# Kernel optimization log

Measured on AMD Instinct MI355X. Metric: run time of the kernel, lower is better.

Reference implementation:

```python
import jax, jax.numpy as jnp
jax.config.update("jax_enable_x64", True)
import numpy as np
import math

N = 100_000   # number of events
D = 4         # feature dim
M = 256       # number of Gaussian centers
E = 10        # ensemble size
SIGMA = 0.1
NORM_CONST = 1.0 / ((2.0 * math.pi) ** (D / 2) * SIGMA ** D)


def setup_inputs() -> dict:
    key = jax.random.key(0)
    k = jax.random.split(key, 6)
    x = jax.random.normal(k[0], (N, D), dtype=jnp.float64)
    centers = jax.random.normal(k[1], (M, D), dtype=jnp.float64)
    coefficients = jax.random.normal(k[2], (M,), dtype=jnp.float64)
    ensemble_probs = jax.random.uniform(k[3], (N, E), dtype=jnp.float64)
    ensemble_norm_probs = jax.random.uniform(k[4], (N, 1), dtype=jnp.float64)
    # small positive weights so 1 - sum(w) stays positive (as in a fitted model)
    weights = 0.05 * jax.random.uniform(k[5], (E,), dtype=jnp.float64)
    return {
        "x": x,
        "ensemble_probs": ensemble_probs,
        "ensemble_norm_probs": ensemble_norm_probs,
        "weights": weights,
        "centers": centers,
        "coefficients": coefficients,
    }


def reference(x, ensemble_probs, ensemble_norm_probs, weights, centers, coefficients):
    # GaussianKernelLayer.get_kernels: pairwise squared distances -> RBF
    diff = x[:, None, :] - centers[None, :, :]          # [N, M, D]
    dist_sq = jnp.sum(diff * diff, axis=2)              # [N, M]
    kern = NORM_CONST * jnp.exp(-0.5 * dist_sq / (SIGMA ** 2))  # [N, M]
    # centered coefficients, contract: einsum('m,Nm->N')
    wc = coefficients - coefficients.mean()
    net_out = kern @ wc                                 # [N]
    # ensemble mixture: w [E,1], w_norm [1,1]
    w = weights[:, None]
    w_norm = 1.0 - jnp.sum(w, axis=0, keepdims=True)
    ensemble = ensemble_probs @ w + ensemble_norm_probs @ w_norm  # [N, 1]
    return (ensemble, net_out)
```

## Files before the change

### kernel.cpp

```cpp
#include <hip/hip_runtime.h>
#include <math.h>

#define NROWS 100000
#define EENS 10

#define NORM_CONST_F 253.30295910584444f
#define EXP2_SCALE (-72.13475204444817f)
#define M2_CONST   (144.26950408889634f)
#define ARG_THRESH (-18.0f)

typedef _Float16 h8 __attribute__((ext_vector_type(8)));
typedef float    f4 __attribute__((ext_vector_type(4)));


__global__ __launch_bounds__(512, 1) void fused_kernel(
    const float* __restrict__ x,
    const float* __restrict__ ensemble_probs,
    const float* __restrict__ ensemble_norm_probs,
    const float* __restrict__ weights,
    const float* __restrict__ centers,
    const float* __restrict__ coefficients,
    float* __restrict__ out)
{
    const int t    = threadIdx.x;
    const int lane = t & 63;
    const int wid  = t >> 6;
    const int wg   = blockIdx.x * 8 + wid;
    if (wg >= NROWS / 32) return;
    const int wbase = wg * 32;

    const int lr = lane & 15;
    const int g  = lane >> 4;

    const float4 cq = ((const float4*)coefficients)[lane];
    float ms = (cq.x + cq.y) + (cq.z + cq.w);
    #pragma unroll
    for (int off = 32; off > 0; off >>= 1) ms += __shfl_down(ms, off, 64);
    const float mean = __builtin_amdgcn_readfirstlane(ms) * (1.0f / 256.0f);

    h8 bf[16]; float As[16], wcv[16];
    #pragma unroll
    for (int T = 0; T < 16; ++T) {
        const float4 cv = ((const float4*)centers)[T * 16 + lr];
        const _Float16 h0 = (_Float16)cv.x, h1 = (_Float16)cv.y,
                       h2 = (_Float16)cv.z, h3 = (_Float16)cv.w;
        const _Float16 l0 = (_Float16)(cv.x - (float)h0),
                       l1 = (_Float16)(cv.y - (float)h1),
                       l2 = (_Float16)(cv.z - (float)h2),
                       l3 = (_Float16)(cv.w - (float)h3);
        h8 b;
        b[0] = h0; b[1] = h1; b[2] = h2; b[3] = h3;
        b[4] = l0; b[5] = l1; b[6] = l2; b[7] = l3;
        bf[T] = b;
        float n2 = cv.x * cv.x;
        n2 = fmaf(cv.y, cv.y, n2);
        n2 = fmaf(cv.z, cv.z, n2);
        n2 = fmaf(cv.w, cv.w, n2);
        As[T]  = EXP2_SCALE * n2;
        wcv[T] = coefficients[T * 16 + lr] - mean;
    }

    const float4 xa = ((const float4*)x)[wbase + lr];
    const float4 xb = ((const float4*)x)[wbase + 16 + lr];

    float hsa = xa.x * xa.x;
    hsa = fmaf(xa.y, xa.y, hsa); hsa = fmaf(xa.z, xa.z, hsa); hsa = fmaf(xa.w, xa.w, hsa);
    hsa *= EXP2_SCALE;
    float hsb = xb.x * xb.x;
    hsb = fmaf(xb.y, xb.y, hsb); hsb = fmaf(xb.z, xb.z, hsb); hsb = fmaf(xb.w, xb.w, hsb);
    hsb *= EXP2_SCALE;

    const float HA0 = __shfl(hsa, g * 4 + 0, 64), HA1 = __shfl(hsa, g * 4 + 1, 64),
                HA2 = __shfl(hsa, g * 4 + 2, 64), HA3 = __shfl(hsa, g * 4 + 3, 64);
    const float HB0 = __shfl(hsb, g * 4 + 0, 64), HB1 = __shfl(hsb, g * 4 + 1, 64),
                HB2 = __shfl(hsb, g * 4 + 2, 64), HB3 = __shfl(hsb, g * 4 + 3, 64);

    const float a0f = (float)(_Float16)xa.x, a1f = (float)(_Float16)xa.y,
                a2f = (float)(_Float16)xa.z, a3f = (float)(_Float16)xa.w;
    const float b0f = (float)(_Float16)xb.x, b1f = (float)(_Float16)xb.y,
                b2f = (float)(_Float16)xb.z, b3f = (float)(_Float16)xb.w;

    const float sa0 = (g == 0) ? a0f : (g == 1) ? (xa.x - a0f) : 0.f;
    const float sa1 = (g == 0) ? a1f : (g == 1) ? (xa.y - a1f) : 0.f;
    const float sa2 = (g == 0) ? a2f : (g == 1) ? (xa.z - a2f) : 0.f;
    const float sa3 = (g == 0) ? a3f : (g == 1) ? (xa.w - a3f) : 0.f;
    const float sb0 = (g == 0) ? b0f : (g == 1) ? (xb.x - b0f) : 0.f;
    const float sb1 = (g == 0) ? b1f : (g == 1) ? (xb.y - b1f) : 0.f;
    const float sb2 = (g == 0) ? b2f : (g == 1) ? (xb.z - b2f) : 0.f;
    const float sb3 = (g == 0) ? b3f : (g == 1) ? (xb.w - b3f) : 0.f;

    h8 afA, afB;
    afA[0] = (_Float16)sa0; afA[1] = (_Float16)sa1; afA[2] = (_Float16)sa2; afA[3] = (_Float16)sa3;
    afA[4] = afA[0]; afA[5] = afA[1]; afA[6] = afA[2]; afA[7] = afA[3];
    afB[0] = (_Float16)sb0; afB[1] = (_Float16)sb1; afB[2] = (_Float16)sb2; afB[3] = (_Float16)sb3;
    afB[4] = afB[0]; afB[5] = afB[1]; afB[6] = afB[2]; afB[7] = afB[3];

    f4 accA = {0.f, 0.f, 0.f, 0.f};
    f4 accB = {0.f, 0.f, 0.f, 0.f};
    const f4 z4 = {0.f, 0.f, 0.f, 0.f};

    #pragma unroll
    for (int T = 0; T < 16; ++T) {
        const f4 dA = __builtin_amdgcn_mfma_f32_16x16x32_f16(afA, bf[T], z4, 0, 0, 0);
        const f4 dB = __builtin_amdgcn_mfma_f32_16x16x32_f16(afB, bf[T], z4, 0, 0, 0);

        const float baseA = As[T];
        const float ra0 = fmaf(M2_CONST, dA[0], HA0 + baseA);
        const float ra1 = fmaf(M2_CONST, dA[1], HA1 + baseA);
        const float ra2 = fmaf(M2_CONST, dA[2], HA2 + baseA);
        const float ra3 = fmaf(M2_CONST, dA[3], HA3 + baseA);
        const float mxa = fmaxf(fmaxf(ra0, ra1), fmaxf(ra2, ra3));
        if (__any(mxa > ARG_THRESH)) {
            const float e0 = __builtin_amdgcn_exp2f(ra0);
            const float e1 = __builtin_amdgcn_exp2f(ra1);
            const float e2 = __builtin_amdgcn_exp2f(ra2);
            const float e3 = __builtin_amdgcn_exp2f(ra3);
            accA[0] = fmaf(e0, wcv[T], accA[0]);
            accA[1] = fmaf(e1, wcv[T], accA[1]);
            accA[2] = fmaf(e2, wcv[T], accA[2]);
            accA[3] = fmaf(e3, wcv[T], accA[3]);
        }

        const float rb0 = fmaf(M2_CONST, dB[0], HB0 + baseA);
        const float rb1 = fmaf(M2_CONST, dB[1], HB1 + baseA);
        const float rb2 = fmaf(M2_CONST, dB[2], HB2 + baseA);
        const float rb3 = fmaf(M2_CONST, dB[3], HB3 + baseA);
        const float mxb = fmaxf(fmaxf(rb0, rb1), fmaxf(rb2, rb3));
        if (__any(mxb > ARG_THRESH)) {
            const float e0 = __builtin_amdgcn_exp2f(rb0);
            const float e1 = __builtin_amdgcn_exp2f(rb1);
            const float e2 = __builtin_amdgcn_exp2f(rb2);
            const float e3 = __builtin_amdgcn_exp2f(rb3);
            accB[0] = fmaf(e0, wcv[T], accB[0]);
            accB[1] = fmaf(e1, wcv[T], accB[1]);
            accB[2] = fmaf(e2, wcv[T], accB[2]);
            accB[3] = fmaf(e3, wcv[T], accB[3]);
        }
    }

    #pragma unroll
    for (int msk = 1; msk <= 8; msk <<= 1) {
        accA[0] += __shfl_xor(accA[0], msk, 64);
        accA[1] += __shfl_xor(accA[1], msk, 64);
        accA[2] += __shfl_xor(accA[2], msk, 64);
        accA[3] += __shfl_xor(accA[3], msk, 64);
        accB[0] += __shfl_xor(accB[0], msk, 64);
        accB[1] += __shfl_xor(accB[1], msk, 64);
        accB[2] += __shfl_xor(accB[2], msk, 64);
        accB[3] += __shfl_xor(accB[3], msk, 64);
    }
    if (lr == 0) {
        const int rbA = wbase + g * 4;
        out[NROWS + rbA + 0] = accA[0] * NORM_CONST_F;
        out[NROWS + rbA + 1] = accA[1] * NORM_CONST_F;
        out[NROWS + rbA + 2] = accA[2] * NORM_CONST_F;
        out[NROWS + rbA + 3] = accA[3] * NORM_CONST_F;
        const int rbB = rbA + 16;
        out[NROWS + rbB + 0] = accB[0] * NORM_CONST_F;
        out[NROWS + rbB + 1] = accB[1] * NORM_CONST_F;
        out[NROWS + rbB + 2] = accB[2] * NORM_CONST_F;
        out[NROWS + rbB + 3] = accB[3] * NORM_CONST_F;
    }

    if (lane < 32) {
        const int r = wbase + lane;
        float wv[EENS];
        float wsum = 0.0f;
        #pragma unroll
        for (int e = 0; e < EENS; ++e) { wv[e] = weights[e]; wsum += wv[e]; }
        float ens = ensemble_norm_probs[r] * (1.0f - wsum);
        const float2* pr = (const float2*)(ensemble_probs + (size_t)r * EENS);
        #pragma unroll
        for (int e2 = 0; e2 < EENS / 2; ++e2) {
            const float2 p = pr[e2];
            ens = fmaf(p.x, wv[2 * e2 + 0], ens);
            ens = fmaf(p.y, wv[2 * e2 + 1], ens);
        }
        out[r] = ens;
    }
}

extern "C" void kernel_launch(void* const* d_in, const int* in_sizes, int n_in,
                              void* d_out, int out_size, void* d_ws, size_t ws_size,
                              hipStream_t stream) {
    const float* x       = (const float*)d_in[0];
    const float* eprobs  = (const float*)d_in[1];
    const float* enorm   = (const float*)d_in[2];
    const float* weights = (const float*)d_in[3];
    const float* centers = (const float*)d_in[4];
    const float* coeffs  = (const float*)d_in[5];
    float* out = (float*)d_out;

    const int waves  = NROWS / 32;
    const int blocks = (waves + 7) / 8;
    fused_kernel<<<blocks, 512, 0, stream>>>(
        x, eprobs, enorm, weights, centers, coeffs, out);
}
```

Measured before the change: 13.93 us.

## Convert to grid-stride persistent waves reusing per-wave center setup across tiles

The kernel now launches a fixed grid of 512 blocks of 256 threads (2048 waves) that loop over the 3125 row tiles of 32 rows, instead of one wave per tile. The per-wave setup (coefficient mean, half-precision center fragments, center norms, centered coefficients, ensemble weights) is computed once and reused across tiles, which amortises that redundant prologue. Launch bounds drop from 512 threads with one-block occupancy to 256. The tile count does not divide evenly over 2048 waves, so some waves run two tiles and others one, which can leave a tail that lengthens the critical path.

```diff
diff --git a/kernel.cpp b/kernel.cpp
--- a/kernel.cpp
+++ b/kernel.cpp
@@ -3,6 +3,8 @@
 
 #define NROWS 100000
 #define EENS 10
+#define NTILES 3125
+#define GWAVES 2048
 
 #define NORM_CONST_F 253.30295910584444f
 #define EXP2_SCALE (-72.13475204444817f)
@@ -13,7 +15,7 @@
 typedef float    f4 __attribute__((ext_vector_type(4)));
 
 
-__global__ __launch_bounds__(512, 1) void fused_kernel(
+__global__ __launch_bounds__(256) void fused_kernel(
     const float* __restrict__ x,
     const float* __restrict__ ensemble_probs,
     const float* __restrict__ ensemble_norm_probs,
@@ -25,12 +27,9 @@
     const int t    = threadIdx.x;
     const int lane = t & 63;
     const int wid  = t >> 6;
-    const int wg   = blockIdx.x * 8 + wid;
-    if (wg >= NROWS / 32) return;
-    const int wbase = wg * 32;
-
-    const int lr = lane & 15;
-    const int g  = lane >> 4;
+    const int gw   = blockIdx.x * 4 + wid;
+    const int lr   = lane & 15;
+    const int g    = lane >> 4;
 
     const float4 cq = ((const float4*)coefficients)[lane];
     float ms = (cq.x + cq.y) + (cq.z + cq.w);
@@ -44,13 +43,12 @@
         const float4 cv = ((const float4*)centers)[T * 16 + lr];
         const _Float16 h0 = (_Float16)cv.x, h1 = (_Float16)cv.y,
                        h2 = (_Float16)cv.z, h3 = (_Float16)cv.w;
-        const _Float16 l0 = (_Float16)(cv.x - (float)h0),
-                       l1 = (_Float16)(cv.y - (float)h1),
-                       l2 = (_Float16)(cv.z - (float)h2),
-                       l3 = (_Float16)(cv.w - (float)h3);
         h8 b;
         b[0] = h0; b[1] = h1; b[2] = h2; b[3] = h3;
-        b[4] = l0; b[5] = l1; b[6] = l2; b[7] = l3;
+        b[4] = (_Float16)(cv.x - (float)h0);
+        b[5] = (_Float16)(cv.y - (float)h1);
+        b[6] = (_Float16)(cv.z - (float)h2);
+        b[7] = (_Float16)(cv.w - (float)h3);
         bf[T] = b;
         float n2 = cv.x * cv.x;
         n2 = fmaf(cv.y, cv.y, n2);
@@ -60,123 +58,121 @@
         wcv[T] = coefficients[T * 16 + lr] - mean;
     }
 
-    const float4 xa = ((const float4*)x)[wbase + lr];
-    const float4 xb = ((const float4*)x)[wbase + 16 + lr];
+    float wv[EENS];
+    float wsum = 0.0f;
+    #pragma unroll
+    for (int e = 0; e < EENS; ++e) { wv[e] = weights[e]; wsum += wv[e]; }
+    const float wnorm = 1.0f - wsum;
 
-    float hsa = xa.x * xa.x;
-    hsa = fmaf(xa.y, xa.y, hsa); hsa = fmaf(xa.z, xa.z, hsa); hsa = fmaf(xa.w, xa.w, hsa);
-    hsa *= EXP2_SCALE;
-    float hsb = xb.x * xb.x;
-    hsb = fmaf(xb.y, xb.y, hsb); hsb = fmaf(xb.z, xb.z, hsb); hsb = fmaf(xb.w, xb.w, hsb);
-    hsb *= EXP2_SCALE;
+    for (int tile = gw; tile < NTILES; tile += GWAVES) {
+        const int wbase = tile * 32;
 
-    const float HA0 = __shfl(hsa, g * 4 + 0, 64), HA1 = __shfl(hsa, g * 4 + 1, 64),
-                HA2 = __shfl(hsa, g * 4 + 2, 64), HA3 = __shfl(hsa, g * 4 + 3, 64);
-    const float HB0 = __shfl(hsb, g * 4 + 0, 64), HB1 = __shfl(hsb, g * 4 + 1, 64),
-                HB2 = __shfl(hsb, g * 4 + 2, 64), HB3 = __shfl(hsb, g * 4 + 3, 64);
+        const float4 xa = ((const float4*)x)[wbase + lr];
+        const float4 xb = ((const float4*)x)[wbase + 16 + lr];
 
-    const float a0f = (float)(_Float16)xa.x, a1f = (float)(_Float16)xa.y,
-                a2f = (float)(_Float16)xa.z, a3f = (float)(_Float16)xa.w;
-    const float b0f = (float)(_Float16)xb.x, b1f = (float)(_Float16)xb.y,
-                b2f = (float)(_Float16)xb.z, b3f = (float)(_Float16)xb.w;
+        float hsa = xa.x * xa.x;
+        hsa = fmaf(xa.y, xa.y, hsa); hsa = fmaf(xa.z, xa.z, hsa); hsa = fmaf(xa.w, xa.w, hsa);
+        hsa *= EXP2_SCALE;
+        float hsb = xb.x * xb.x;
+        hsb = fmaf(xb.y, xb.y, hsb); hsb = fmaf(xb.z, xb.z, hsb); hsb = fmaf(xb.w, xb.w, hsb);
+        hsb *= EXP2_SCALE;
 
-    const float sa0 = (g == 0) ? a0f : (g == 1) ? (xa.x - a0f) : 0.f;
-    const float sa1 = (g == 0) ? a1f : (g == 1) ? (xa.y - a1f) : 0.f;
-    const float sa2 = (g == 0) ? a2f : (g == 1) ? (xa.z - a2f) : 0.f;
-    const float sa3 = (g == 0) ? a3f : (g == 1) ? (xa.w - a3f) : 0.f;
-    const float sb0 = (g == 0) ? b0f : (g == 1) ? (xb.x - b0f) : 0.f;
-    const float sb1 = (g == 0) ? b1f : (g == 1) ? (xb.y - b1f) : 0.f;
-    const float sb2 = (g == 0) ? b2f : (g == 1) ? (xb.z - b2f) : 0.f;
-    const float sb3 = (g == 0) ? b3f : (g == 1) ? (xb.w - b3f) : 0.f;
+        const float HA0 = __shfl(hsa, g * 4 + 0, 64), HA1 = __shfl(hsa, g * 4 + 1, 64),
+                    HA2 = __shfl(hsa, g * 4 + 2, 64), HA3 = __shfl(hsa, g * 4 + 3, 64);
+        const float HB0 = __shfl(hsb, g * 4 + 0, 64), HB1 = __shfl(hsb, g * 4 + 1, 64),
+                    HB2 = __shfl(hsb, g * 4 + 2, 64), HB3 = __shfl(hsb, g * 4 + 3, 64);
 
-    h8 afA, afB;
-    afA[0] = (_Float16)sa0; afA[1] = (_Float16)sa1; afA[2] = (_Float16)sa2; afA[3] = (_Float16)sa3;
-    afA[4] = afA[0]; afA[5] = afA[1]; afA[6] = afA[2]; afA[7] = afA[3];
-    afB[0] = (_Float16)sb0; afB[1] = (_Float16)sb1; afB[2] = (_Float16)sb2; afB[3] = (_Float16)sb3;
-    afB[4] = afB[0]; afB[5] = afB[1]; afB[6] = afB[2]; afB[7] = afB[3];
+        const float a0f = (float)(_Float16)xa.x, a1f = (float)(_Float16)xa.y,
+                    a2f = (float)(_Float16)xa.z, a3f = (float)(_Float16)xa.w;
+        const float b0f = (float)(_Float16)xb.x, b1f = (float)(_Float16)xb.y,
+                    b2f = (float)(_Float16)xb.z, b3f = (float)(_Float16)xb.w;
 
-    f4 accA = {0.f, 0.f, 0.f, 0.f};
-    f4 accB = {0.f, 0.f, 0.f, 0.f};
-    const f4 z4 = {0.f, 0.f, 0.f, 0.f};
+        const float sa0 = (g == 0) ? a0f : (g == 1) ? (xa.x - a0f) : 0.f;
+        const float sa1 = (g == 0) ? a1f : (g == 1) ? (xa.y - a1f) : 0.f;
+        const float sa2 = (g == 0) ? a2f : (g == 1) ? (xa.z - a2f) : 0.f;
+        const float sa3 = (g == 0) ? a3f : (g == 1) ? (xa.w - a3f) : 0.f;
+        const float sb0 = (g == 0) ? b0f : (g == 1) ? (xb.x - b0f) : 0.f;
+        const float sb1 = (g == 0) ? b1f : (g == 1) ? (xb.y - b1f) : 0.f;
+        const float sb2 = (g == 0) ? b2f : (g == 1) ? (xb.z - b2f) : 0.f;
+        const float sb3 = (g == 0) ? b3f : (g == 1) ? (xb.w - b3f) : 0.f;
 
-    #pragma unroll
-    for (int T = 0; T < 16; ++T) {
-        const f4 dA = __builtin_amdgcn_mfma_f32_16x16x32_f16(afA, bf[T], z4, 0, 0, 0);
-        const f4 dB = __builtin_amdgcn_mfma_f32_16x16x32_f16(afB, bf[T], z4, 0, 0, 0);
+        h8 afA, afB;
+        afA[0] = (_Float16)sa0; afA[1] = (_Float16)sa1; afA[2] = (_Float16)sa2; afA[3] = (_Float16)sa3;
+        afA[4] = afA[0]; afA[5] = afA[1]; afA[6] = afA[2]; afA[7] = afA[3];
+        afB[0] = (_Float16)sb0; afB[1] = (_Float16)sb1; afB[2] = (_Float16)sb2; afB[3] = (_Float16)sb3;
+        afB[4] = afB[0]; afB[5] = afB[1]; afB[6] = afB[2]; afB[7] = afB[3];
 
-        const float baseA = As[T];
-        const float ra0 = fmaf(M2_CONST, dA[0], HA0 + baseA);
-        const float ra1 = fmaf(M2_CONST, dA[1], HA1 + baseA);
-        const float ra2 = fmaf(M2_CONST, dA[2], HA2 + baseA);
-        const float ra3 = fmaf(M2_CONST, dA[3], HA3 + baseA);
-        const float mxa = fmaxf(fmaxf(ra0, ra1), fmaxf(ra2, ra3));
-        if (__any(mxa > ARG_THRESH)) {
-            const float e0 = __builtin_amdgcn_exp2f(ra0);
-            const float e1 = __builtin_amdgcn_exp2f(ra1);
-            const float e2 = __builtin_amdgcn_exp2f(ra2);
-            const float e3 = __builtin_amdgcn_exp2f(ra3);
-            accA[0] = fmaf(e0, wcv[T], accA[0]);
-            accA[1] = fmaf(e1, wcv[T], accA[1]);
-            accA[2] = fmaf(e2, wcv[T], accA[2]);
-            accA[3] = fmaf(e3, wcv[T], accA[3]);
+        f4 accA = {0.f, 0.f, 0.f, 0.f};
+        f4 accB = {0.f, 0.f, 0.f, 0.f};
+        const f4 z4 = {0.f, 0.f, 0.f, 0.f};
+
+        #pragma unroll
+        for (int T = 0; T < 16; ++T) {
+            const f4 dA = __builtin_amdgcn_mfma_f32_16x16x32_f16(afA, bf[T], z4, 0, 0, 0);
+            const f4 dB = __builtin_amdgcn_mfma_f32_16x16x32_f16(afB, bf[T], z4, 0, 0, 0);
+
+            const float baseA = As[T];
+            const float ra0 = fmaf(M2_CONST, dA[0], HA0 + baseA);
+            const float ra1 = fmaf(M2_CONST, dA[1], HA1 + baseA);
+            const float ra2 = fmaf(M2_CONST, dA[2], HA2 + baseA);
+            const float ra3 = fmaf(M2_CONST, dA[3], HA3 + baseA);
+            const float mxa = fmaxf(fmaxf(ra0, ra1), fmaxf(ra2, ra3));
+            if (__any(mxa > ARG_THRESH)) {
+                accA[0] = fmaf(__builtin_amdgcn_exp2f(ra0), wcv[T], accA[0]);
+                accA[1] = fmaf(__builtin_amdgcn_exp2f(ra1), wcv[T], accA[1]);
+                accA[2] = fmaf(__builtin_amdgcn_exp2f(ra2), wcv[T], accA[2]);
+                accA[3] = fmaf(__builtin_amdgcn_exp2f(ra3), wcv[T], accA[3]);
+            }
+
+            const float rb0 = fmaf(M2_CONST, dB[0], HB0 + baseA);
+            const float rb1 = fmaf(M2_CONST, dB[1], HB1 + baseA);
+            const float rb2 = fmaf(M2_CONST, dB[2], HB2 + baseA);
+            const float rb3 = fmaf(M2_CONST, dB[3], HB3 + baseA);
+            const float mxb = fmaxf(fmaxf(rb0, rb1), fmaxf(rb2, rb3));
+            if (__any(mxb > ARG_THRESH)) {
+                accB[0] = fmaf(__builtin_amdgcn_exp2f(rb0), wcv[T], accB[0]);
+                accB[1] = fmaf(__builtin_amdgcn_exp2f(rb1), wcv[T], accB[1]);
+                accB[2] = fmaf(__builtin_amdgcn_exp2f(rb2), wcv[T], accB[2]);
+                accB[3] = fmaf(__builtin_amdgcn_exp2f(rb3), wcv[T], accB[3]);
+            }
         }
 
-        const float rb0 = fmaf(M2_CONST, dB[0], HB0 + baseA);
-        const float rb1 = fmaf(M2_CONST, dB[1], HB1 + baseA);
-        const float rb2 = fmaf(M2_CONST, dB[2], HB2 + baseA);
-        const float rb3 = fmaf(M2_CONST, dB[3], HB3 + baseA);
-        const float mxb = fmaxf(fmaxf(rb0, rb1), fmaxf(rb2, rb3));
-        if (__any(mxb > ARG_THRESH)) {
-            const float e0 = __builtin_amdgcn_exp2f(rb0);
-            const float e1 = __builtin_amdgcn_exp2f(rb1);
-            const float e2 = __builtin_amdgcn_exp2f(rb2);
-            const float e3 = __builtin_amdgcn_exp2f(rb3);
-            accB[0] = fmaf(e0, wcv[T], accB[0]);
-            accB[1] = fmaf(e1, wcv[T], accB[1]);
-            accB[2] = fmaf(e2, wcv[T], accB[2]);
-            accB[3] = fmaf(e3, wcv[T], accB[3]);
+        #pragma unroll
+        for (int msk = 1; msk <= 8; msk <<= 1) {
+            accA[0] += __shfl_xor(accA[0], msk, 64);
+            accA[1] += __shfl_xor(accA[1], msk, 64);
+            accA[2] += __shfl_xor(accA[2], msk, 64);
+            accA[3] += __shfl_xor(accA[3], msk, 64);
+            accB[0] += __shfl_xor(accB[0], msk, 64);
+            accB[1] += __shfl_xor(accB[1], msk, 64);
+            accB[2] += __shfl_xor(accB[2], msk, 64);
+            accB[3] += __shfl_xor(accB[3], msk, 64);
         }
-    }
+        if (lr == 0) {
+            const int rbA = wbase + g * 4;
+            out[NROWS + rbA + 0] = accA[0] * NORM_CONST_F;
+            out[NROWS + rbA + 1] = accA[1] * NORM_CONST_F;
+            out[NROWS + rbA + 2] = accA[2] * NORM_CONST_F;
+            out[NROWS + rbA + 3] = accA[3] * NORM_CONST_F;
+            const int rbB = rbA + 16;
+            out[NROWS + rbB + 0] = accB[0] * NORM_CONST_F;
+            out[NROWS + rbB + 1] = accB[1] * NORM_CONST_F;
+            out[NROWS + rbB + 2] = accB[2] * NORM_CONST_F;
+            out[NROWS + rbB + 3] = accB[3] * NORM_CONST_F;
+        }
 
-    #pragma unroll
-    for (int msk = 1; msk <= 8; msk <<= 1) {
-        accA[0] += __shfl_xor(accA[0], msk, 64);
-        accA[1] += __shfl_xor(accA[1], msk, 64);
-        accA[2] += __shfl_xor(accA[2], msk, 64);
-        accA[3] += __shfl_xor(accA[3], msk, 64);
-        accB[0] += __shfl_xor(accB[0], msk, 64);
-        accB[1] += __shfl_xor(accB[1], msk, 64);
-        accB[2] += __shfl_xor(accB[2], msk, 64);
-        accB[3] += __shfl_xor(accB[3], msk, 64);
-    }
-    if (lr == 0) {
-        const int rbA = wbase + g * 4;
-        out[NROWS + rbA + 0] = accA[0] * NORM_CONST_F;
-        out[NROWS + rbA + 1] = accA[1] * NORM_CONST_F;
-        out[NROWS + rbA + 2] = accA[2] * NORM_CONST_F;
-        out[NROWS + rbA + 3] = accA[3] * NORM_CONST_F;
-        const int rbB = rbA + 16;
-        out[NROWS + rbB + 0] = accB[0] * NORM_CONST_F;
-        out[NROWS + rbB + 1] = accB[1] * NORM_CONST_F;
-        out[NROWS + rbB + 2] = accB[2] * NORM_CONST_F;
-        out[NROWS + rbB + 3] = accB[3] * NORM_CONST_F;
-    }
-
-    if (lane < 32) {
-        const int r = wbase + lane;
-        float wv[EENS];
-        float wsum = 0.0f;
-        #pragma unroll
-        for (int e = 0; e < EENS; ++e) { wv[e] = weights[e]; wsum += wv[e]; }
-        float ens = ensemble_norm_probs[r] * (1.0f - wsum);
-        const float2* pr = (const float2*)(ensemble_probs + (size_t)r * EENS);
-        #pragma unroll
-        for (int e2 = 0; e2 < EENS / 2; ++e2) {
-            const float2 p = pr[e2];
-            ens = fmaf(p.x, wv[2 * e2 + 0], ens);
-            ens = fmaf(p.y, wv[2 * e2 + 1], ens);
+        if (lane < 32) {
+            const int r = wbase + lane;
+            float ens = ensemble_norm_probs[r] * wnorm;
+            const float2* pr = (const float2*)(ensemble_probs + (size_t)r * EENS);
+            #pragma unroll
+            for (int e2 = 0; e2 < EENS / 2; ++e2) {
+                const float2 p = pr[e2];
+                ens = fmaf(p.x, wv[2 * e2 + 0], ens);
+                ens = fmaf(p.y, wv[2 * e2 + 1], ens);
+            }
+            out[r] = ens;
         }
-        out[r] = ens;
     }
 }
 
@@ -191,8 +187,6 @@
     const float* coeffs  = (const float*)d_in[5];
     float* out = (float*)d_out;
 
-    const int waves  = NROWS / 32;
-    const int blocks = (waves + 7) / 8;
-    fused_kernel<<<blocks, 512, 0, stream>>>(
+    fused_kernel<<<512, 256, 0, stream>>>(
         x, eprobs, enorm, weights, centers, coeffs, out);
 }
```

Result: slower. 14.77 us (+6.1%).
